# Performance work log

Hardware: AMD Instinct MI355X
Metric: run time of the kernel (lower is better)

Reference implementation:

```python
import jax, jax.numpy as jnp
import numpy as np

L, B, D = 512, 4, 1024          # seq(atoms), batch, embed dim
H, DH = 16, 64                  # heads, head dim
FF = 4096                       # ffn hidden
HP = 32                         # encoder_pair_embed_dim
K = 256                         # pbc-expanded atoms


def _ln(x, g, b):
    m = x.mean(-1, keepdims=True)
    v = x.var(-1, keepdims=True)
    return (x - m) / jnp.sqrt(v + 1e-5) * g + b


def _rope(x, pos):
    # x: [S,B,H,DH], pos: [B,S]
    inv_freq = 1.0 / (10000.0 ** (jnp.arange(0, DH, 2, dtype=jnp.float32) / DH))
    ang = pos.astype(jnp.float32)[..., None] * inv_freq          # [B,S,DH/2]
    cos = jnp.cos(ang).transpose(1, 0, 2)[:, :, None, :]          # [S,B,1,DH/2]
    sin = jnp.sin(ang).transpose(1, 0, 2)[:, :, None, :]
    x1, x2 = jnp.split(x, 2, axis=-1)
    return jnp.concatenate([x1 * cos - x2 * sin, x1 * sin + x2 * cos], axis=-1)


def setup_inputs() -> dict:
    key = jax.random.key(0)
    ks = jax.random.split(key, 12)
    s = 0.02
    return dict(
        x=jax.random.normal(ks[0], (L, B, D), jnp.float32),
        x_pair=jax.random.normal(ks[1], (L, L + K, B, HP), jnp.float32),
        padding_mask=jnp.zeros((B, L), bool),
        expand_mask=jnp.zeros((B, K), bool),
        position_ids=jnp.tile(jnp.arange(L, dtype=jnp.int32)[None, :], (B, 1)),
        outcell_index=jax.random.randint(ks[2], (B, K), 0, L, dtype=jnp.int32),
        wq=jax.random.normal(ks[3], (D, D), jnp.float32) * s,
        wk=jax.random.normal(ks[4], (D, D), jnp.float32) * s,
        wv=jax.random.normal(ks[5], (D, D), jnp.float32) * s,
        wo=jax.random.normal(ks[6], (D, D), jnp.float32) * s,
        fc1=jax.random.normal(ks[7], (D, FF), jnp.float32) * s,
        fc2=jax.random.normal(ks[8], (FF, D), jnp.float32) * s,
        top_ln_g=jnp.ones((D,), jnp.float32), top_ln_b=jnp.zeros((D,), jnp.float32),
        mid_ln_g=jnp.ones((D,), jnp.float32), mid_ln_b=jnp.zeros((D,), jnp.float32),
        pair_ln_g=jnp.ones((D,), jnp.float32), pair_ln_b=jnp.zeros((D,), jnp.float32),
        pair_w1=jax.random.normal(ks[9], (D, 2 * HP), jnp.float32) * s,
        pair_w2=jax.random.normal(ks[10], (2 * HP, HP), jnp.float32) * s,
    )


def reference(x, x_pair, padding_mask, expand_mask, position_ids, outcell_index,
              wq, wk, wv, wo, fc1, fc2,
              top_ln_g, top_ln_b, mid_ln_g, mid_ln_b,
              pair_ln_g, pair_ln_b, pair_w1, pair_w2):
    barange = jnp.arange(B)
    # ---- self-attention block (pre-LN, RoPE, pbc-expanded keys/values) ----
    residual = x
    h = _ln(x, top_ln_g, top_ln_b)                               # [L,B,D]
    h_exp = h[outcell_index.T, barange[None, :], :]               # [K,B,D] gather along L per batch
    kv_src = jnp.concatenate([h, h_exp], axis=0)                  # [L+K,B,D]
    q = (h @ wq).reshape(L, B, H, DH)
    k = (kv_src @ wk).reshape(L + K, B, H, DH)
    v = (kv_src @ wv).reshape(L + K, B, H, DH)
    pos_exp = position_ids[barange[:, None], outcell_index]       # [B,K]
    pos_k = jnp.concatenate([position_ids, pos_exp], axis=1)      # [B,L+K]
    q = _rope(q, position_ids)
    k = _rope(k, pos_k)
    scores = jnp.einsum('lbhd,kbhd->bhlk', q, k) / np.sqrt(DH)    # [B,H,L,L+K]
    kp_mask = jnp.concatenate([padding_mask, expand_mask], axis=1)  # [B,L+K]
    scores = jnp.where(kp_mask[:, None, None, :], -1e9, scores)
    attn = jax.nn.softmax(scores, axis=-1)
    o = jnp.einsum('bhlk,kbhd->lbhd', attn, v).reshape(L, B, D) @ wo
    x = residual + o
    # ---- FFN block ----
    residual = x
    h = _ln(x, mid_ln_g, mid_ln_b)
    x = residual + jax.nn.gelu(h @ fc1, approximate=False) @ fc2
    # ---- pair outer product ----
    x_p_i = jax.nn.silu(_ln(x, pair_ln_g, pair_ln_b) @ pair_w1) @ pair_w2   # [L,B,HP]
    expand_x_p_i = x_p_i[outcell_index.T, barange[None, :], :]              # [K,B,HP]
    x_p_j = jnp.concatenate([x_p_i, expand_x_p_i], axis=0)                  # [L+K,B,HP]
    x_pair = x_pair + jnp.einsum('lbh,kbh->lkbh', x_p_i, x_p_j)             # [L,L+K,B,HP]
    return x, x_pair
```

## Files before the change

### kernel.cpp

```cpp
#include <hip/hip_runtime.h>
#include <math.h>


typedef __bf16 bf16x8 __attribute__((ext_vector_type(8)));
typedef float f32x4 __attribute__((ext_vector_type(4)));

__device__ __forceinline__ unsigned short f2bf(float f) {
  unsigned u = __float_as_uint(f);
  u = (u + 0x7fffu + ((u >> 16) & 1u)) >> 16;
  return (unsigned short)u;
}
__device__ __forceinline__ float bf2f(unsigned short s) {
  return __uint_as_float(((unsigned)s) << 16);
}

__device__ __forceinline__ void gload_lds16(const void* g, void* l) {
  __builtin_amdgcn_global_load_lds(
      (__attribute__((address_space(1))) void*)g,
      (__attribute__((address_space(3))) void*)l, 16, 0, 0);
}

__global__ __launch_bounds__(256) void transpose_all(
    const float* __restrict__ wq, const float* __restrict__ wk, const float* __restrict__ wv,
    const float* __restrict__ wo, const float* __restrict__ fc1, const float* __restrict__ fc2,
    unsigned short* __restrict__ qkvT, unsigned short* __restrict__ woT,
    unsigned short* __restrict__ fc1T, unsigned short* __restrict__ fc2T) {
  int id = blockIdx.x;
  const float* W; unsigned short* WT; int Kd, Nd, n0, k0;
  if (id < 2048) {
    int which = id >> 9, lid = id & 511;
    W = which == 0 ? wq : (which == 1 ? wk : (which == 2 ? wv : wo));
    WT = which < 3 ? qkvT + (long)which * 1024 * 1024 : woT;
    Kd = 1024; Nd = 1024;
    k0 = (lid >> 5) * 64; n0 = (lid & 31) * 32;
  } else if (id < 4096) {
    int lid = id - 2048;
    W = fc1; WT = fc1T; Kd = 1024; Nd = 4096;
    k0 = (lid >> 7) * 64; n0 = (lid & 127) * 32;
  } else {
    int lid = id - 4096;
    W = fc2; WT = fc2T; Kd = 4096; Nd = 1024;
    k0 = (lid >> 5) * 64; n0 = (lid & 31) * 32;
  }
  __shared__ float tile[64][33];
  const int tx = threadIdx.x, ty = threadIdx.y;
#pragma unroll
  for (int j = 0; j < 64; j += 8)
    tile[ty + j][tx] = W[(long)(k0 + ty + j) * Nd + n0 + tx];
  __syncthreads();
#pragma unroll
  for (int i = 0; i < 32; i += 8) {
    ushort2 o;
    o.x = f2bf(tile[2 * tx][ty + i]);
    o.y = f2bf(tile[2 * tx + 1][ty + i]);
    *(ushort2*)&WT[(long)(n0 + ty + i) * Kd + k0 + 2 * tx] = o;
  }
}

__global__ __launch_bounds__(256) void ln_bf16(
    const float* __restrict__ X, unsigned short* __restrict__ Y,
    const float* __restrict__ g, const float* __restrict__ bb) {
  const int row = blockIdx.x, t = threadIdx.x;
  const float* xr = X + (long)row * 1024;
  float v[4]; float s = 0.f, ss = 0.f;
#pragma unroll
  for (int i = 0; i < 4; i++) { v[i] = xr[t + 256 * i]; s += v[i]; ss += v[i] * v[i]; }
#pragma unroll
  for (int o = 32; o > 0; o >>= 1) { s += __shfl_down(s, o); ss += __shfl_down(ss, o); }
  __shared__ float red[8];
  const int wave = t >> 6, lane = t & 63;
  if (lane == 0) { red[wave] = s; red[4 + wave] = ss; }
  __syncthreads();
  s = red[0] + red[1] + red[2] + red[3];
  ss = red[4] + red[5] + red[6] + red[7];
  const float mean = s * (1.f / 1024.f);
  const float rstd = rsqrtf(ss * (1.f / 1024.f) - mean * mean + 1e-5f);
#pragma unroll
  for (int i = 0; i < 4; i++) {
    const int c = t + 256 * i;
    Y[(long)row * 1024 + c] = f2bf((v[i] - mean) * rstd * g[c] + bb[c]);
  }
}

__global__ __launch_bounds__(256) void red_ln(
    const float* __restrict__ p0, const float* __restrict__ p1,
    const float* __restrict__ R, float* __restrict__ Xout,
    const float* __restrict__ g, const float* __restrict__ bb,
    unsigned short* __restrict__ Y) {
  const int row = blockIdx.x, t = threadIdx.x;
  const long base = (long)row * 1024;
  float v[4]; float s = 0.f, ss = 0.f;
#pragma unroll
  for (int i = 0; i < 4; i++) {
    const int c = t + 256 * i;
    float val = p0[base + c] + p1[base + c] + R[base + c];
    Xout[base + c] = val;
    v[i] = val; s += val; ss += val * val;
  }
#pragma unroll
  for (int o = 32; o > 0; o >>= 1) { s += __shfl_down(s, o); ss += __shfl_down(ss, o); }
  __shared__ float red[8];
  const int wave = t >> 6, lane = t & 63;
  if (lane == 0) { red[wave] = s; red[4 + wave] = ss; }
  __syncthreads();
  s = red[0] + red[1] + red[2] + red[3];
  ss = red[4] + red[5] + red[6] + red[7];
  const float mean = s * (1.f / 1024.f);
  const float rstd = rsqrtf(ss * (1.f / 1024.f) - mean * mean + 1e-5f);
#pragma unroll
  for (int i = 0; i < 4; i++) {
    const int c = t + 256 * i;
    Y[base + c] = f2bf((v[i] - mean) * rstd * g[c] + bb[c]);
  }
}

__global__ __launch_bounds__(256) void red_ln_pair(
    const float* __restrict__ p0, const float* __restrict__ p1,
    const float* __restrict__ R, float* __restrict__ Xout,
    const float* __restrict__ g, const float* __restrict__ bb,
    const float* __restrict__ w1, const float* __restrict__ w2,
    float* __restrict__ xpi) {
  const int row = blockIdx.x, t = threadIdx.x;
  const long base = (long)row * 1024;
  __shared__ float lnrow[1024];
  __shared__ float red[8];
  __shared__ float red2[64][4];
  __shared__ float s1[64];
  float v[4]; float s = 0.f, ss = 0.f;
#pragma unroll
  for (int i = 0; i < 4; i++) {
    const int c = t + 256 * i;
    float val = p0[base + c] + p1[base + c] + R[base + c];
    Xout[base + c] = val;
    v[i] = val; s += val; ss += val * val;
  }
#pragma unroll
  for (int o = 32; o > 0; o >>= 1) { s += __shfl_down(s, o); ss += __shfl_down(ss, o); }
  const int wave = t >> 6, lane = t & 63;
  if (lane == 0) { red[wave] = s; red[4 + wave] = ss; }
  __syncthreads();
  s = red[0] + red[1] + red[2] + red[3];
  ss = red[4] + red[5] + red[6] + red[7];
  const float mean = s * (1.f / 1024.f);
  const float rstd = rsqrtf(ss * (1.f / 1024.f) - mean * mean + 1e-5f);
#pragma unroll
  for (int i = 0; i < 4; i++) {
    const int c = t + 256 * i;
    lnrow[c] = (v[i] - mean) * rstd * g[c] + bb[c];
  }
  __syncthreads();
  const int c = t & 63, qt = t >> 6;
  float acc = 0.f;
  for (int k = qt * 256; k < qt * 256 + 256; k++)
    acc += lnrow[k] * w1[k * 64 + c];
  red2[c][qt] = acc;
  __syncthreads();
  if (t < 64) {
    float vv = red2[t][0] + red2[t][1] + red2[t][2] + red2[t][3];
    s1[t] = vv / (1.f + __expf(-vv));
  }
  __syncthreads();
  if (t < 32) {
    float o = 0.f;
    for (int k = 0; k < 64; k++) o += s1[k] * w2[k * 32 + t];
    xpi[(long)row * 32 + t] = o;
  }
}

__global__ __launch_bounds__(256) void gather_kv(unsigned short* kv, const int* __restrict__ oc) {
  int idx = blockIdx.x * 256 + threadIdx.x;
  int col4 = idx & 255;
  int r = idx >> 8;
  int j = r >> 2, b = r & 3;
  int src = oc[b * 256 + j] * 4 + b;
  ((ushort4*)kv)[((512 + j) * 4 + b) * 256 + col4] = ((const ushort4*)kv)[src * 256 + col4];
}

template <int EPI>
__global__ __launch_bounds__(256) void gemm_nt(
    const unsigned short* __restrict__ A, const unsigned short* __restrict__ BT,
    void* __restrict__ Cout, const float* __restrict__ R, int M, int N, int Kd) {
  __shared__ __align__(16) unsigned short As[128 * 32];
  __shared__ __align__(16) unsigned short Bs[128 * 32];
  const int t = threadIdx.x;
  const int wave = t >> 6, lane = t & 63;
  const int m0 = blockIdx.y * 128, n0 = blockIdx.x * 128;
  const int wr = wave >> 1, wc = wave & 1;
  const int lr = lane & 15, lg = lane >> 4;

  f32x4 acc[4][4] = {};

  const int srow = 32 * wave + (lane >> 2);
  const int schunk = (lane & 3) * 8;
  const unsigned short* Ag = A + (long)(m0 + srow) * Kd + schunk;
  const unsigned short* Bg = BT + (long)(n0 + srow) * Kd + schunk;
  unsigned short* AsW = &As[(32 * wave) * 32];
  unsigned short* BsW = &Bs[(32 * wave) * 32];

  for (int k0 = 0; k0 < Kd; k0 += 32) {
    __syncthreads();
    gload_lds16(Ag + k0, AsW);
    gload_lds16(Ag + k0 + 16 * (long)Kd, AsW + 16 * 32);
    gload_lds16(Bg + k0, BsW);
    gload_lds16(Bg + k0 + 16 * (long)Kd, BsW + 16 * 32);
    asm volatile("s_waitcnt vmcnt(0)" ::: "memory");
    __syncthreads();

    bf16x8 af[4], bfr[4];
#pragma unroll
    for (int mf = 0; mf < 4; mf++)
      af[mf] = *(const bf16x8*)&As[(64 * wr + 16 * mf + lr) * 32 + lg * 8];
#pragma unroll
    for (int nf = 0; nf < 4; nf++)
      bfr[nf] = *(const bf16x8*)&Bs[(64 * wc + 16 * nf + lr) * 32 + lg * 8];
#pragma unroll
    for (int mf = 0; mf < 4; mf++)
#pragma unroll
      for (int nf = 0; nf < 4; nf++)
        acc[mf][nf] = __builtin_amdgcn_mfma_f32_16x16x32_bf16(af[mf], bfr[nf], acc[mf][nf], 0, 0, 0);
  }

#pragma unroll
  for (int mf = 0; mf < 4; mf++)
#pragma unroll
    for (int nf = 0; nf < 4; nf++)
#pragma unroll
      for (int r = 0; r < 4; r++) {
        const int row = m0 + 64 * wr + 16 * mf + 4 * lg + r;
        const int col = n0 + 64 * wc + 16 * nf + lr;
        const long off = (long)row * N + col;
        float v = acc[mf][nf][r];
        if constexpr (EPI == 1) {
          ((float*)Cout)[off] = v + R[off];
        } else if constexpr (EPI == 2) {
          float gl = 0.5f * v * (1.0f + erff(v * 0.70710678118654752f));
          ((unsigned short*)Cout)[off] = f2bf(gl);
        } else if constexpr (EPI == 3) {
          ((unsigned short*)Cout)[off] = f2bf(v);
        } else {
          ((float*)Cout)[off] = v;
        }
      }
}

__global__ __launch_bounds__(256) void gemm_qkv(
    const unsigned short* __restrict__ A, const unsigned short* __restrict__ BT,
    unsigned short* __restrict__ Cout) {
  constexpr int N = 3072, Kd = 1024;
  int bid = blockIdx.x;
  int mt, nt;
  if (bid < 384) { mt = bid / 24; nt = bid % 24; }
  else { int rem = bid - 384; mt = 16 + (rem >> 4); nt = 8 + (rem & 15); }
  const int m0 = mt * 128, n0 = nt * 128;

  __shared__ __align__(16) unsigned short As[128 * 32];
  __shared__ __align__(16) unsigned short Bs[128 * 32];
  const int t = threadIdx.x;
  const int wave = t >> 6, lane = t & 63;
  const int wr = wave >> 1, wc = wave & 1;
  const int lr = lane & 15, lg = lane >> 4;

  f32x4 acc[4][4] = {};

  const int srow = 32 * wave + (lane >> 2);
  const int schunk = (lane & 3) * 8;
  const unsigned short* Ag = A + (long)(m0 + srow) * Kd + schunk;
  const unsigned short* Bg = BT + (long)(n0 + srow) * Kd + schunk;
  unsigned short* AsW = &As[(32 * wave) * 32];
  unsigned short* BsW = &Bs[(32 * wave) * 32];

  for (int k0 = 0; k0 < Kd; k0 += 32) {
    __syncthreads();
    gload_lds16(Ag + k0, AsW);
    gload_lds16(Ag + k0 + 16 * (long)Kd, AsW + 16 * 32);
    gload_lds16(Bg + k0, BsW);
    gload_lds16(Bg + k0 + 16 * (long)Kd, BsW + 16 * 32);
    asm volatile("s_waitcnt vmcnt(0)" ::: "memory");
    __syncthreads();

    bf16x8 af[4], bfr[4];
#pragma unroll
    for (int mf = 0; mf < 4; mf++)
      af[mf] = *(const bf16x8*)&As[(64 * wr + 16 * mf + lr) * 32 + lg * 8];
#pragma unroll
    for (int nf = 0; nf < 4; nf++)
      bfr[nf] = *(const bf16x8*)&Bs[(64 * wc + 16 * nf + lr) * 32 + lg * 8];
#pragma unroll
    for (int mf = 0; mf < 4; mf++)
#pragma unroll
      for (int nf = 0; nf < 4; nf++)
        acc[mf][nf] = __builtin_amdgcn_mfma_f32_16x16x32_bf16(af[mf], bfr[nf], acc[mf][nf], 0, 0, 0);
  }

#pragma unroll
  for (int mf = 0; mf < 4; mf++)
#pragma unroll
    for (int nf = 0; nf < 4; nf++)
#pragma unroll
      for (int r = 0; r < 4; r++) {
        const int row = m0 + 64 * wr + 16 * mf + 4 * lg + r;
        const int col = n0 + 64 * wc + 16 * nf + lr;
        Cout[(long)row * N + col] = f2bf(acc[mf][nf][r]);
      }
}

__global__ __launch_bounds__(256) void gemm_nt_splitk(
    const unsigned short* __restrict__ A, const unsigned short* __restrict__ BT,
    float* __restrict__ Cp, int M, int N, int Kd) {
  const int kh = Kd >> 1;
  const long kbase = (long)blockIdx.z * kh;
  const unsigned short* A2 = A + kbase;
  const unsigned short* B2 = BT + kbase;
  float* Cz = Cp + (long)blockIdx.z * M * N;

  __shared__ __align__(16) unsigned short As[128 * 32];
  __shared__ __align__(16) unsigned short Bs[128 * 32];
  const int t = threadIdx.x;
  const int wave = t >> 6, lane = t & 63;
  const int m0 = blockIdx.y * 128, n0 = blockIdx.x * 128;
  const int wr = wave >> 1, wc = wave & 1;
  const int lr = lane & 15, lg = lane >> 4;

  f32x4 acc[4][4] = {};

  const int srow = 32 * wave + (lane >> 2);
  const int schunk = (lane & 3) * 8;
  const unsigned short* Ag = A2 + (long)(m0 + srow) * Kd + schunk;
  const unsigned short* Bg = B2 + (long)(n0 + srow) * Kd + schunk;
  unsigned short* AsW = &As[(32 * wave) * 32];
  unsigned short* BsW = &Bs[(32 * wave) * 32];

  for (int k0 = 0; k0 < kh; k0 += 32) {
    __syncthreads();
    gload_lds16(Ag + k0, AsW);
    gload_lds16(Ag + k0 + 16 * (long)Kd, AsW + 16 * 32);
    gload_lds16(Bg + k0, BsW);
    gload_lds16(Bg + k0 + 16 * (long)Kd, BsW + 16 * 32);
    asm volatile("s_waitcnt vmcnt(0)" ::: "memory");
    __syncthreads();

    bf16x8 af[4], bfr[4];
#pragma unroll
    for (int mf = 0; mf < 4; mf++)
      af[mf] = *(const bf16x8*)&As[(64 * wr + 16 * mf + lr) * 32 + lg * 8];
#pragma unroll
    for (int nf = 0; nf < 4; nf++)
      bfr[nf] = *(const bf16x8*)&Bs[(64 * wc + 16 * nf + lr) * 32 + lg * 8];
#pragma unroll
    for (int mf = 0; mf < 4; mf++)
#pragma unroll
      for (int nf = 0; nf < 4; nf++)
        acc[mf][nf] = __builtin_amdgcn_mfma_f32_16x16x32_bf16(af[mf], bfr[nf], acc[mf][nf], 0, 0, 0);
  }

#pragma unroll
  for (int mf = 0; mf < 4; mf++)
#pragma unroll
    for (int nf = 0; nf < 4; nf++)
#pragma unroll
      for (int r = 0; r < 4; r++) {
        const int row = m0 + 64 * wr + 16 * mf + 4 * lg + r;
        const int col = n0 + 64 * wc + 16 * nf + lr;
        Cz[(long)row * N + col] = acc[mf][nf][r];
      }
}

__global__ __launch_bounds__(256) void rope_split2(
    const unsigned short* __restrict__ QKV, const int* __restrict__ pos_ids,
    const int* __restrict__ oc,
    unsigned short* __restrict__ qb, unsigned short* __restrict__ kbh) {
  int idx = blockIdx.x * 256 + threadIdx.x;
  bool isq = idx < 1048576;
  int rp = isq ? idx : idx - 1048576;
  int p = rp & 511;
  int row = rp >> 9;
  int hh = p >> 5, dp = p & 31;
  int s = row >> 2, b = row & 3;
  int pos = isq ? pos_ids[b * 512 + s]
                : ((s < 512) ? pos_ids[b * 512 + s]
                             : pos_ids[b * 512 + oc[b * 256 + s - 512]]);
  const unsigned short* src = QKV + (long)row * 3072 + (isq ? 0 : 1024) + hh * 64 + dp;
  float x1 = bf2f(src[0]), x2 = bf2f(src[32]);
  float invf = exp2f((float)dp * -0.41524101186091903f);
  float ang = (float)pos * invf;
  float sn = sinf(ang), cs = cosf(ang);
  float o1 = x1 * cs - x2 * sn, o2 = x1 * sn + x2 * cs;
  if (isq) {
    unsigned short* dst = qb + ((long)(b * 16 + hh) * 512 + s) * 64 + dp;
    dst[0] = f2bf(o1 * 0.125f); dst[32] = f2bf(o2 * 0.125f);
  } else {
    unsigned short* dst = kbh + ((long)(b * 16 + hh) * 768 + s) * 64 + dp;
    dst[0] = f2bf(o1); dst[32] = f2bf(o2);
  }
}

__global__ __launch_bounds__(256) void v_transpose(
    const unsigned short* __restrict__ QKV, unsigned short* __restrict__ vth) {
  const int kt = blockIdx.x, bh = blockIdx.y;
  const int b = bh >> 4, h = bh & 15;
  __shared__ unsigned short tile[64][72];
  const int t = threadIdx.x;
  const int key = t >> 2, c = t & 3;
  const unsigned short* src = QKV + ((long)(kt * 64 + key) * 4 + b) * 3072 + 2048 + h * 64 + c * 16;
#pragma unroll
  for (int j = 0; j < 16; j++) tile[c * 16 + j][key] = src[j];
  __syncthreads();
  const int d = t >> 2;
  unsigned short* dst = vth + ((long)bh * 64 + d) * 768 + kt * 64 + c * 16;
  *(uint4*)dst = *(const uint4*)&tile[d][c * 16];
  *(uint4*)(dst + 8) = *(const uint4*)&tile[d][c * 16 + 8];
}

__global__ __launch_bounds__(512) void att_mfma(
    const unsigned short* __restrict__ qb, const unsigned short* __restrict__ kbh,
    const unsigned short* __restrict__ vth,
    const unsigned char* __restrict__ pad_mask, const unsigned char* __restrict__ exp_mask,
    unsigned short* __restrict__ o_bf) {
  const int bh = blockIdx.y, b = bh >> 4, h = bh & 15;
  const int q0 = blockIdx.x * 128;
  const int t = threadIdx.x, wave = t >> 6, lane = t & 63;
  const int lr = lane & 15, lg = lane >> 4;

  __shared__ __align__(16) unsigned short Ps[8][16][72];
  __shared__ float maskAdd[768];

  for (int i = t; i < 768; i += 512)
    maskAdd[i] = ((i < 512) ? pad_mask[b * 512 + i] : exp_mask[b * 256 + i - 512]) ? -1e9f : 0.f;

  const unsigned short* qrow = qb + ((long)bh * 512 + q0 + wave * 16 + lr) * 64;
  const bf16x8 aq0 = *(const bf16x8*)(qrow + lg * 8);
  const bf16x8 aq1 = *(const bf16x8*)(qrow + 32 + lg * 8);
  __syncthreads();

  float m_run[4] = {-1e30f, -1e30f, -1e30f, -1e30f};
  float l_run[4] = {0.f, 0.f, 0.f, 0.f};
  f32x4 Oacc[4] = {};

  const unsigned short* kb0 = kbh + (long)bh * 768 * 64;
  const unsigned short* vb0 = vth + (long)bh * 64 * 768;

  for (int kt = 0; kt < 12; ++kt) {
    float sv[4][4];
#pragma unroll
    for (int nf = 0; nf < 4; nf++) {
      const unsigned short* kr = kb0 + (long)(kt * 64 + nf * 16 + lr) * 64;
      f32x4 z = {};
      bf16x8 b0 = *(const bf16x8*)(kr + lg * 8);
      bf16x8 b1 = *(const bf16x8*)(kr + 32 + lg * 8);
      z = __builtin_amdgcn_mfma_f32_16x16x32_bf16(aq0, b0, z, 0, 0, 0);
      z = __builtin_amdgcn_mfma_f32_16x16x32_bf16(aq1, b1, z, 0, 0, 0);
      float ma = maskAdd[kt * 64 + nf * 16 + lr];
#pragma unroll
      for (int r = 0; r < 4; r++) sv[nf][r] = z[r] + ma;
    }
    float mnew[4], scale[4], rs[4];
#pragma unroll
    for (int r = 0; r < 4; r++) {
      float tm = fmaxf(fmaxf(sv[0][r], sv[1][r]), fmaxf(sv[2][r], sv[3][r]));
      tm = fmaxf(tm, __shfl_xor(tm, 1));
      tm = fmaxf(tm, __shfl_xor(tm, 2));
      tm = fmaxf(tm, __shfl_xor(tm, 4));
      tm = fmaxf(tm, __shfl_xor(tm, 8));
      mnew[r] = fmaxf(m_run[r], tm);
      scale[r] = __expf(m_run[r] - mnew[r]);
      m_run[r] = mnew[r];
      rs[r] = 0.f;
    }
#pragma unroll
    for (int nf = 0; nf < 4; nf++)
#pragma unroll
      for (int r = 0; r < 4; r++) {
        float p = __expf(sv[nf][r] - mnew[r]);
        rs[r] += p;
        Ps[wave][lg * 4 + r][nf * 16 + lr] = f2bf(p);
      }
#pragma unroll
    for (int r = 0; r < 4; r++) {
      float x = rs[r];
      x += __shfl_xor(x, 1); x += __shfl_xor(x, 2);
      x += __shfl_xor(x, 4); x += __shfl_xor(x, 8);
      l_run[r] = l_run[r] * scale[r] + x;
#pragma unroll
      for (int nf = 0; nf < 4; nf++) Oacc[nf][r] *= scale[r];
    }
    bf16x8 ap0 = *(const bf16x8*)&Ps[wave][lr][lg * 8];
    bf16x8 ap1 = *(const bf16x8*)&Ps[wave][lr][32 + lg * 8];
#pragma unroll
    for (int nf = 0; nf < 4; nf++) {
      const unsigned short* vr = vb0 + (long)(nf * 16 + lr) * 768 + kt * 64;
      bf16x8 b0 = *(const bf16x8*)(vr + lg * 8);
      bf16x8 b1 = *(const bf16x8*)(vr + 32 + lg * 8);
      Oacc[nf] = __builtin_amdgcn_mfma_f32_16x16x32_bf16(ap0, b0, Oacc[nf], 0, 0, 0);
      Oacc[nf] = __builtin_amdgcn_mfma_f32_16x16x32_bf16(ap1, b1, Oacc[nf], 0, 0, 0);
    }
  }

#pragma unroll
  for (int r = 0; r < 4; r++) {
    float inv = 1.0f / l_run[r];
    int l = q0 + wave * 16 + lg * 4 + r;
#pragma unroll
    for (int nf = 0; nf < 4; nf++)
      o_bf[(((long)l * 4 + b) * 16 + h) * 64 + nf * 16 + lr] = f2bf(Oacc[nf][r] * inv);
  }
}

__global__ __launch_bounds__(256) void pair_update(
    const float* __restrict__ x_pair, const float* __restrict__ xpi,
    const int* __restrict__ oc, float* __restrict__ out) {
  int idx4 = blockIdx.x * 256 + threadIdx.x;
  int h4 = idx4 & 7;
  int lkb = idx4 >> 3;
  int b = lkb & 3;
  int lk = lkb >> 2;
  int kk = lk % 768;
  int l = lk / 768;
  int src = (kk < 512) ? kk : oc[b * 256 + kk - 512];
  float4 pv = ((const float4*)x_pair)[idx4];
  float4 a = ((const float4*)xpi)[(l * 4 + b) * 8 + h4];
  float4 bb = ((const float4*)xpi)[(src * 4 + b) * 8 + h4];
  float4 o;
  o.x = pv.x + a.x * bb.x; o.y = pv.y + a.y * bb.y;
  o.z = pv.z + a.z * bb.z; o.w = pv.w + a.w * bb.w;
  ((float4*)out)[idx4] = o;
}

extern "C" void kernel_launch(void* const* d_in, const int* in_sizes, int n_in,
                              void* d_out, int out_size, void* d_ws, size_t ws_size,
                              hipStream_t stream) {
  const float* x        = (const float*)d_in[0];
  const float* x_pair   = (const float*)d_in[1];
  const unsigned char* pad_mask = (const unsigned char*)d_in[2];
  const unsigned char* exp_mask = (const unsigned char*)d_in[3];
  const int* pos_ids    = (const int*)d_in[4];
  const int* oc         = (const int*)d_in[5];
  const float* wq  = (const float*)d_in[6];
  const float* wk  = (const float*)d_in[7];
  const float* wv  = (const float*)d_in[8];
  const float* wo  = (const float*)d_in[9];
  const float* fc1 = (const float*)d_in[10];
  const float* fc2 = (const float*)d_in[11];
  const float* tln_g = (const float*)d_in[12];
  const float* tln_b = (const float*)d_in[13];
  const float* mln_g = (const float*)d_in[14];
  const float* mln_b = (const float*)d_in[15];
  const float* pln_g = (const float*)d_in[16];
  const float* pln_b = (const float*)d_in[17];
  const float* w1 = (const float*)d_in[18];
  const float* w2 = (const float*)d_in[19];

  char* wsp = (char*)d_ws;
  size_t off = 0;
  auto alloc = [&](size_t bytes) -> void* {
    void* p = wsp + off;
    off = (off + bytes + 255) & ~(size_t)255;
    return p;
  };
  unsigned short* qkvT = (unsigned short*)alloc(3072LL * 1024 * 2);
  unsigned short* woT  = (unsigned short*)alloc(1024LL * 1024 * 2);
  unsigned short* fc1T = (unsigned short*)alloc(4096LL * 1024 * 2);
  unsigned short* fc2T = (unsigned short*)alloc(1024LL * 4096 * 2);
  unsigned short* kvb  = (unsigned short*)alloc(3072LL * 1024 * 2);
  unsigned short* QKVb = (unsigned short*)alloc(3072LL * 3072 * 2);
  unsigned short* qb   = (unsigned short*)alloc(64LL * 512 * 64 * 2);
  unsigned short* kbh  = (unsigned short*)alloc(64LL * 768 * 64 * 2);
  unsigned short* vth  = (unsigned short*)alloc(64LL * 64 * 768 * 2);
  unsigned short* obf  = (unsigned short*)alloc(2048LL * 1024 * 2);
  float* x1            = (float*)alloc(2048LL * 1024 * 4);
  unsigned short* h2   = (unsigned short*)alloc(2048LL * 1024 * 2);
  unsigned short* gbf  = (unsigned short*)alloc(2048LL * 4096 * 2);
  float* xpi           = (float*)alloc(2048LL * 32 * 4);
  float* pp            = (float*)alloc(2LL * 2048 * 1024 * 4);
  (void)ws_size; (void)in_sizes; (void)n_in; (void)out_size;

  dim3 tb(32, 8);
  transpose_all<<<6144, tb, 0, stream>>>(wq, wk, wv, wo, fc1, fc2,
                                         qkvT, woT, fc1T, fc2T);

  ln_bf16<<<2048, 256, 0, stream>>>(x, kvb, tln_g, tln_b);
  gather_kv<<<1024, 256, 0, stream>>>(kvb, oc);

  gemm_qkv<<<512, 256, 0, stream>>>(kvb, qkvT, QKVb);

  rope_split2<<<10240, 256, 0, stream>>>(QKVb, pos_ids, oc, qb, kbh);
  v_transpose<<<dim3(12, 64), 256, 0, stream>>>(QKVb, vth);

  att_mfma<<<dim3(4, 64), 512, 0, stream>>>(qb, kbh, vth, pad_mask, exp_mask, obf);

  gemm_nt_splitk<<<dim3(8, 16, 2), 256, 0, stream>>>(obf, woT, pp, 2048, 1024, 1024);
  red_ln<<<2048, 256, 0, stream>>>(pp, pp + 2097152, x, x1, mln_g, mln_b, h2);

  gemm_nt<2><<<dim3(32, 16), 256, 0, stream>>>(h2, fc1T, gbf, nullptr, 2048, 4096, 1024);

  gemm_nt_splitk<<<dim3(8, 16, 2), 256, 0, stream>>>(gbf, fc2T, pp, 2048, 1024, 4096);
  red_ln_pair<<<2048, 256, 0, stream>>>(pp, pp + 2097152, x1, (float*)d_out,
                                        pln_g, pln_b, w1, w2, xpi);

  pair_update<<<49152, 256, 0, stream>>>(x_pair, xpi, oc, (float*)d_out + 2097152);
}
```

Before: 318.2 us.

## Fuse RoPE and head-split layout into QKV GEMM epilogue

The QKV GEMM epilogue now applies rotary embedding, the 1/sqrt(dh) scale and the per-head scatter directly into the q/k head-major buffers, and writes V head-major for the transpose kernel. This removes the separate rope_split2 kernel and the full QKV intermediate round trip through memory. A small pos_prep kernel precomputes key positions, and the fast __sincosf intrinsic replaces sinf/cosf, which may lose accuracy for large angles. The epilogue stores are scattered 2-byte writes, which may coalesce poorly.

New measurement: 330.9 us. 4.0% more time.

```diff
diff --git a/kernel.cpp b/kernel.cpp
--- a/kernel.cpp
+++ b/kernel.cpp
@@ -176,6 +176,14 @@
   ((ushort4*)kv)[((512 + j) * 4 + b) * 256 + col4] = ((const ushort4*)kv)[src * 256 + col4];
 }
 
+__global__ __launch_bounds__(256) void pos_prep(
+    const int* __restrict__ pos_ids, const int* __restrict__ oc, int* __restrict__ posk) {
+  int i = blockIdx.x * 256 + threadIdx.x;
+  int s = i >> 2, b = i & 3;
+  posk[i] = (s < 512) ? pos_ids[b * 512 + s]
+                      : pos_ids[b * 512 + oc[b * 256 + s - 512]];
+}
+
 template <int EPI>
 __global__ __launch_bounds__(256) void gemm_nt(
     const unsigned short* __restrict__ A, const unsigned short* __restrict__ BT,
@@ -245,8 +253,10 @@
 
 __global__ __launch_bounds__(256) void gemm_qkv(
     const unsigned short* __restrict__ A, const unsigned short* __restrict__ BT,
-    unsigned short* __restrict__ Cout) {
-  constexpr int N = 3072, Kd = 1024;
+    const int* __restrict__ posk,
+    unsigned short* __restrict__ qb, unsigned short* __restrict__ kbh,
+    unsigned short* __restrict__ vbh) {
+  constexpr int Kd = 1024;
   int bid = blockIdx.x;
   int mt, nt;
   if (bid < 384) { mt = bid / 24; nt = bid % 24; }
@@ -292,16 +302,49 @@
         acc[mf][nf] = __builtin_amdgcn_mfma_f32_16x16x32_bf16(af[mf], bfr[nf], acc[mf][nf], 0, 0, 0);
   }
 
-#pragma unroll
-  for (int mf = 0; mf < 4; mf++)
-#pragma unroll
-    for (int nf = 0; nf < 4; nf++)
+  const int sec = (nt < 8) ? 0 : (nt < 16 ? 1 : 2);
+  const int h = 2 * (nt - sec * 8) + wc;
+  const int sb = (m0 >> 2) + 16 * wr + lg;
+
+  if (sec == 2) {
+#pragma unroll
+    for (int mf = 0; mf < 4; mf++) {
+      const int s = sb + 4 * mf;
 #pragma unroll
       for (int r = 0; r < 4; r++) {
-        const int row = m0 + 64 * wr + 16 * mf + 4 * lg + r;
-        const int col = n0 + 64 * wc + 16 * nf + lr;
-        Cout[(long)row * N + col] = f2bf(acc[mf][nf][r]);
+        unsigned short* dst = vbh + ((long)(r * 16 + h) * 768 + s) * 64 + lr;
+#pragma unroll
+        for (int nf = 0; nf < 4; nf++)
+          dst[16 * nf] = f2bf(acc[mf][nf][r]);
       }
+    }
+  } else {
+    const float cfr = 0.41524101186091903f;
+    const float invf0 = exp2f(-(float)lr * cfr);
+    const float invf1 = exp2f(-(float)(lr + 16) * cfr);
+    const float qs = (sec == 0) ? 0.125f : 1.0f;
+    const int Ls = (sec == 0) ? 512 : 768;
+    unsigned short* base = (sec == 0) ? qb : kbh;
+#pragma unroll
+    for (int mf = 0; mf < 4; mf++) {
+      const int s = sb + 4 * mf;
+      const int4 pv = *(const int4*)&posk[s * 4];
+#pragma unroll
+      for (int r = 0; r < 4; r++) {
+        const int pos = r == 0 ? pv.x : (r == 1 ? pv.y : (r == 2 ? pv.z : pv.w));
+        float s0, c0, s1, c1;
+        __sincosf((float)pos * invf0, &s0, &c0);
+        __sincosf((float)pos * invf1, &s1, &c1);
+        const float x1a = acc[mf][0][r], x1b = acc[mf][1][r];
+        const float x2a = acc[mf][2][r], x2b = acc[mf][3][r];
+        unsigned short* dst = base + ((long)(r * 16 + h) * Ls + s) * 64 + lr;
+        dst[0]  = f2bf((x1a * c0 - x2a * s0) * qs);
+        dst[16] = f2bf((x1b * c1 - x2b * s1) * qs);
+        dst[32] = f2bf((x1a * s0 + x2a * c0) * qs);
+        dst[48] = f2bf((x1b * s1 + x2b * c1) * qs);
+      }
+    }
+  }
 }
 
 __global__ __launch_bounds__(256) void gemm_nt_splitk(
@@ -365,43 +408,13 @@
       }
 }
 
-__global__ __launch_bounds__(256) void rope_split2(
-    const unsigned short* __restrict__ QKV, const int* __restrict__ pos_ids,
-    const int* __restrict__ oc,
-    unsigned short* __restrict__ qb, unsigned short* __restrict__ kbh) {
-  int idx = blockIdx.x * 256 + threadIdx.x;
-  bool isq = idx < 1048576;
-  int rp = isq ? idx : idx - 1048576;
-  int p = rp & 511;
-  int row = rp >> 9;
-  int hh = p >> 5, dp = p & 31;
-  int s = row >> 2, b = row & 3;
-  int pos = isq ? pos_ids[b * 512 + s]
-                : ((s < 512) ? pos_ids[b * 512 + s]
-                             : pos_ids[b * 512 + oc[b * 256 + s - 512]]);
-  const unsigned short* src = QKV + (long)row * 3072 + (isq ? 0 : 1024) + hh * 64 + dp;
-  float x1 = bf2f(src[0]), x2 = bf2f(src[32]);
-  float invf = exp2f((float)dp * -0.41524101186091903f);
-  float ang = (float)pos * invf;
-  float sn = sinf(ang), cs = cosf(ang);
-  float o1 = x1 * cs - x2 * sn, o2 = x1 * sn + x2 * cs;
-  if (isq) {
-    unsigned short* dst = qb + ((long)(b * 16 + hh) * 512 + s) * 64 + dp;
-    dst[0] = f2bf(o1 * 0.125f); dst[32] = f2bf(o2 * 0.125f);
-  } else {
-    unsigned short* dst = kbh + ((long)(b * 16 + hh) * 768 + s) * 64 + dp;
-    dst[0] = f2bf(o1); dst[32] = f2bf(o2);
-  }
-}
-
 __global__ __launch_bounds__(256) void v_transpose(
-    const unsigned short* __restrict__ QKV, unsigned short* __restrict__ vth) {
+    const unsigned short* __restrict__ vbh, unsigned short* __restrict__ vth) {
   const int kt = blockIdx.x, bh = blockIdx.y;
-  const int b = bh >> 4, h = bh & 15;
   __shared__ unsigned short tile[64][72];
   const int t = threadIdx.x;
   const int key = t >> 2, c = t & 3;
-  const unsigned short* src = QKV + ((long)(kt * 64 + key) * 4 + b) * 3072 + 2048 + h * 64 + c * 16;
+  const unsigned short* src = vbh + ((long)bh * 768 + kt * 64 + key) * 64 + c * 16;
 #pragma unroll
   for (int j = 0; j < 16; j++) tile[c * 16 + j][key] = src[j];
   __syncthreads();
@@ -561,9 +574,10 @@
   unsigned short* fc1T = (unsigned short*)alloc(4096LL * 1024 * 2);
   unsigned short* fc2T = (unsigned short*)alloc(1024LL * 4096 * 2);
   unsigned short* kvb  = (unsigned short*)alloc(3072LL * 1024 * 2);
-  unsigned short* QKVb = (unsigned short*)alloc(3072LL * 3072 * 2);
+  int* posk            = (int*)alloc(3072LL * 4);
   unsigned short* qb   = (unsigned short*)alloc(64LL * 512 * 64 * 2);
   unsigned short* kbh  = (unsigned short*)alloc(64LL * 768 * 64 * 2);
+  unsigned short* vbh  = (unsigned short*)alloc(64LL * 768 * 64 * 2);
   unsigned short* vth  = (unsigned short*)alloc(64LL * 64 * 768 * 2);
   unsigned short* obf  = (unsigned short*)alloc(2048LL * 1024 * 2);
   float* x1            = (float*)alloc(2048LL * 1024 * 4);
@@ -579,11 +593,11 @@
 
   ln_bf16<<<2048, 256, 0, stream>>>(x, kvb, tln_g, tln_b);
   gather_kv<<<1024, 256, 0, stream>>>(kvb, oc);
-
-  gemm_qkv<<<512, 256, 0, stream>>>(kvb, qkvT, QKVb);
-
-  rope_split2<<<10240, 256, 0, stream>>>(QKVb, pos_ids, oc, qb, kbh);
-  v_transpose<<<dim3(12, 64), 256, 0, stream>>>(QKVb, vth);
+  pos_prep<<<12, 256, 0, stream>>>(pos_ids, oc, posk);
+
+  gemm_qkv<<<512, 256, 0, stream>>>(kvb, qkvT, posk, qb, kbh, vbh);
+
+  v_transpose<<<dim3(12, 64), 256, 0, stream>>>(vbh, vth);
 
   att_mfma<<<dim3(4, 64), 512, 0, stream>>>(qb, kbh, vth, pad_mask, exp_mask, obf);
 
```
